# Optimization experiments

Measured on AMD Instinct MI355X. Metric: run time of the kernel, lower is better.

## Reference

```python
import jax, jax.numpy as jnp
import numpy as np

BN_EPS = 1e-5

def _conv3x3(x, w):
    # x: [N,C,H,W], w: [O,I,3,3], stride 1, padding 1, no bias
    return jax.lax.conv_general_dilated(
        x, w, window_strides=(1, 1), padding=((1, 1), (1, 1)),
        dimension_numbers=("NCHW", "OIHW", "NCHW"))

def _batchnorm(x, gamma, beta):
    # training-mode BN: batch statistics over (N,H,W)
    mean = jnp.mean(x, axis=(0, 2, 3), keepdims=True)
    var = jnp.mean(jnp.square(x - mean), axis=(0, 2, 3), keepdims=True)
    inv = jax.lax.rsqrt(var + BN_EPS)
    g = gamma.reshape(1, -1, 1, 1)
    b = beta.reshape(1, -1, 1, 1)
    return (x - mean) * inv * g + b

def setup_inputs() -> dict:
    key = jax.random.key(0)
    ks = jax.random.split(key, 3)
    x = jax.random.normal(ks[0], (32, 64, 128, 128), dtype=jnp.float32)
    # He-style scaled 3x3 conv kernels
    w1 = jax.random.normal(ks[1], (64, 64, 3, 3), dtype=jnp.float32) * (2.0 / (64 * 9)) ** 0.5
    w2 = jax.random.normal(ks[2], (64, 64, 3, 3), dtype=jnp.float32) * (2.0 / (64 * 9)) ** 0.5
    return {
        "x": x, "w1": w1, "w2": w2,
        "bn1_gamma": jnp.ones((64,), jnp.float32),
        "bn1_beta": jnp.zeros((64,), jnp.float32),
        "bn2_gamma": jnp.ones((64,), jnp.float32),
        "bn2_beta": jnp.zeros((64,), jnp.float32),
    }

def reference(x, w1, w2, bn1_gamma, bn1_beta, bn2_gamma, bn2_beta):
    out = _batchnorm(_conv3x3(x, w1), bn1_gamma, bn1_beta)
    out = _conv3x3(out, w2)
    out = out + x  # option 'A', stride=1, planes[2]==planes[0] -> identity shortcut
    return _batchnorm(out, bn2_gamma, bn2_beta)
```

## Files before the change

kernel.cpp:

```cpp
#include <hip/hip_runtime.h>
#include <hip/hip_bf16.h>

#define NB 32
#define CH 64
#define HH 128
#define WW 128
#define HW (HH*WW)
#define CHW (CH*HW)
#define NCHW (NB*CHW)
#define CNT_PER_CH ((float)(NB*HW))
#define SLOTS 256

typedef __attribute__((ext_vector_type(8)))  short short8;
typedef __attribute__((ext_vector_type(16))) float f32x16;

__device__ __forceinline__ unsigned short f2bf(float f) {
  unsigned u = __builtin_bit_cast(unsigned, f);
  u += 0x7fffu + ((u >> 16) & 1u);
  return (unsigned short)(u >> 16);
}

__global__ __launch_bounds__(256) void t1_pack(const float* __restrict__ x,
                                               unsigned short* __restrict__ xb) {
  __shared__ __align__(16) unsigned short tmp[CH * WW];
  const int bid = blockIdx.x;
  const int tid = threadIdx.x;
  const float* src = x + (size_t)(bid >> 7) * CHW + (size_t)(bid & 127) * WW;
  for (int i = tid; i < 2048; i += 256) {
    const int ci = i >> 5, wq = i & 31;
    const float4 v = *(const float4*)(src + (size_t)ci * HW + wq * 4);
    unsigned short* d = &tmp[ci * WW + wq * 4];
    d[0] = f2bf(v.x); d[1] = f2bf(v.y); d[2] = f2bf(v.z); d[3] = f2bf(v.w);
  }
  __syncthreads();
  unsigned short* dst = xb + (size_t)bid * 8192;
  for (int i = tid; i < 1024; i += 256) {
    const int cb = i >> 7, w = i & 127;
    const unsigned short* s = &tmp[cb * 8 * WW + w];
    uint4 o;
    o.x = (unsigned)s[0]      | ((unsigned)s[WW]     << 16);
    o.y = (unsigned)s[2*WW]   | ((unsigned)s[3*WW]   << 16);
    o.z = (unsigned)s[4*WW]   | ((unsigned)s[5*WW]   << 16);
    o.w = (unsigned)s[6*WW]   | ((unsigned)s[7*WW]   << 16);
    *(uint4*)(dst + ((size_t)cb * WW + w) * 8) = o;
  }
}

__global__ __launch_bounds__(256) void pack_w(const float* __restrict__ w,
                                              const float* __restrict__ s1,
                                              const float* __restrict__ b1,
                                              unsigned short* __restrict__ wpk,
                                              float* __restrict__ tabs) {
  const int tid = threadIdx.x;
  for (int idx = tid; idx < 36864; idx += 256) {
    const int f = idx >> 9, l = (idx >> 3) & 63, r = idx & 7;
    const int m = f & 1, kq = (f >> 1) & 3, t = f >> 3;
    const int co = (l & 31) + 32 * m;
    const int ci = kq * 16 + (l >> 5) * 8 + r;
    float v = w[co * 576 + ci * 9 + t];
    if (s1) v *= s1[ci];
    wpk[idx] = f2bf(v);
  }
  if (tabs != nullptr && tid < 64) {
    const int co = tid;
    float tb[9];
    for (int t = 0; t < 9; ++t) {
      float a = 0.f;
      for (int ci = 0; ci < 64; ++ci) a += w[co * 576 + ci * 9 + t] * b1[ci];
      tb[t] = a;
    }
    tabs[0*64+co] = tb[0]+tb[1]+tb[2]+tb[3]+tb[4]+tb[5]+tb[6]+tb[7]+tb[8];
    tabs[1*64+co] = tb[0]+tb[1]+tb[2];
    tabs[2*64+co] = tb[6]+tb[7]+tb[8];
    tabs[3*64+co] = tb[0]+tb[3]+tb[6];
    tabs[4*64+co] = tb[2]+tb[5]+tb[8];
    tabs[5*64+co] = tb[0]; tabs[6*64+co] = tb[2];
    tabs[7*64+co] = tb[6]; tabs[8*64+co] = tb[8];
  }
}

template <bool IS2>
__global__ __launch_bounds__(64, 3)
void conv_stream(const unsigned short* __restrict__ inb,
                 const unsigned short* __restrict__ wpack,
                 const float* __restrict__ tabs,
                 const float* __restrict__ resid,
                 unsigned short* __restrict__ outb,
                 float* __restrict__ outf,
                 float* __restrict__ psum, float* __restrict__ psq) {
  const int b = blockIdx.x;
  const int vid = ((b & 7) << 11) | (b >> 3);
  const int seg = vid & 3;
  const int h   = (vid >> 2) & 127;
  const int n   = vid >> 9;
  const int lane = threadIdx.x;
  const int half = lane >> 5, lp = lane & 31;
  const int px = (seg << 5) + lp;

  f32x16 acc0 = {}; f32x16 acc1 = {};
  const unsigned short* nbase = inb + (size_t)n * (128 * 8192);

#pragma unroll
  for (int kh = 0; kh < 3; ++kh) {
    const int hr = h + kh - 1;
    if ((unsigned)hr >= 128u) continue;
    const unsigned short* rb = nbase + (size_t)hr * 8192;
#pragma unroll
    for (int kw = 0; kw < 3; ++kw) {
      const int pxs = px + kw - 1;
      const bool wok = (unsigned)pxs < 128u;
      const int pxc = pxs < 0 ? 0 : (pxs > 127 ? 127 : pxs);
#pragma unroll
      for (int kq = 0; kq < 4; ++kq) {
        const int cb = (kq << 1) + half;
        short8 bf = *(const short8*)(rb + ((size_t)cb << 10) + ((size_t)pxc << 3));
        short8 zz = {};
        if (!wok) bf = zz;
        const int f = (((kh * 3 + kw) << 2) + kq) << 1;
        const short8 w0 = *(const short8*)(wpack + ((size_t)f << 9) + ((size_t)lane << 3));
        const short8 w1 = *(const short8*)(wpack + ((size_t)(f + 1) << 9) + ((size_t)lane << 3));
        acc0 = __builtin_amdgcn_mfma_f32_32x32x16_bf16(w0, bf, acc0, 0, 0, 0);
        acc1 = __builtin_amdgcn_mfma_f32_32x32x16_bf16(w1, bf, acc1, 0, 0, 0);
      }
    }
  }

  if (!IS2) {
    unsigned short* dst = outb + (size_t)(n * 128 + h) * 8192;
#pragma unroll
    for (int m = 0; m < 2; ++m) {
      const f32x16& a = m ? acc1 : acc0;
#pragma unroll
      for (int rq = 0; rq < 4; ++rq) {
        uint2 pk;
        pk.x = (unsigned)f2bf(a[rq*4+0]) | ((unsigned)f2bf(a[rq*4+1]) << 16);
        pk.y = (unsigned)f2bf(a[rq*4+2]) | ((unsigned)f2bf(a[rq*4+3]) << 16);
        *(uint2*)(dst + (((size_t)(rq + (m << 2))) << 10) + ((size_t)px << 3) + (half << 2)) = pk;
      }
    }
  } else {
    const bool bh0 = (h == 0), bh1 = (h == 127);
    const bool bw0 = (px == 0), bw1 = (px == 127);
#pragma unroll
    for (int m = 0; m < 2; ++m) {
      f32x16& a = m ? acc1 : acc0;
#pragma unroll
      for (int r = 0; r < 16; ++r) {
        const int co = (r & 3) + ((r >> 2) << 3) + (half << 2) + (m << 5);
        float tb = tabs[co];
        if (bh0) tb -= tabs[64 + co];
        if (bh1) tb -= tabs[128 + co];
        if (bw0) tb -= tabs[192 + co];
        if (bw1) tb -= tabs[256 + co];
        if (bh0 && bw0) tb += tabs[320 + co];
        if (bh0 && bw1) tb += tabs[384 + co];
        if (bh1 && bw0) tb += tabs[448 + co];
        if (bh1 && bw1) tb += tabs[512 + co];
        const size_t oi = (((size_t)(n * 64 + co)) * 128 + h) * 128 + px;
        const float v = a[r] + tb + resid[oi];
        outf[oi] = v;
        a[r] = v;
      }
    }
  }

  const int slot = vid & (SLOTS - 1);
#pragma unroll
  for (int m = 0; m < 2; ++m) {
    const f32x16& a = m ? acc1 : acc0;
#pragma unroll
    for (int r = 0; r < 16; ++r) {
      float s = a[r], q = a[r] * a[r];
      s += __shfl_xor(s, 1);  q += __shfl_xor(q, 1);
      s += __shfl_xor(s, 2);  q += __shfl_xor(q, 2);
      s += __shfl_xor(s, 4);  q += __shfl_xor(q, 4);
      s += __shfl_xor(s, 8);  q += __shfl_xor(q, 8);
      s += __shfl_xor(s, 16); q += __shfl_xor(q, 16);
      if (lp == 0) {
        const int co = (r & 3) + ((r >> 2) << 3) + (half << 2) + (m << 5);
        atomicAdd(&psum[slot * 64 + co], s);
        atomicAdd(&psq [slot * 64 + co], q);
      }
    }
  }
}

__global__ __launch_bounds__(256)
void finalize_bn(const float* __restrict__ psum, const float* __restrict__ psq,
                 const float* __restrict__ gamma, const float* __restrict__ beta,
                 float* __restrict__ scale, float* __restrict__ bias) {
  __shared__ float ls[4][64], lq[4][64];
  const int c = threadIdx.x & 63, sg = threadIdx.x >> 6;
  float s = 0.f, q = 0.f;
  for (int i = sg * (SLOTS / 4); i < (sg + 1) * (SLOTS / 4); ++i) {
    s += psum[(size_t)i * 64 + c];
    q += psq[(size_t)i * 64 + c];
  }
  ls[sg][c] = s; lq[sg][c] = q;
  __syncthreads();
  if (threadIdx.x < 64) {
    s = ls[0][c] + ls[1][c] + ls[2][c] + ls[3][c];
    q = lq[0][c] + lq[1][c] + lq[2][c] + lq[3][c];
    const float mean = s * (1.0f / CNT_PER_CH);
    const float var  = q * (1.0f / CNT_PER_CH) - mean * mean;
    const float inv  = rsqrtf(var + 1e-5f);
    const float sc   = inv * gamma[c];
    scale[c] = sc;
    bias[c]  = beta[c] - mean * sc;
  }
}

__global__ __launch_bounds__(256)
void apply_bn_k(float* __restrict__ out,
                const float* __restrict__ scale, const float* __restrict__ bias) {
  __shared__ float sc[CH], bs[CH];
  if (threadIdx.x < CH) { sc[threadIdx.x] = scale[threadIdx.x]; bs[threadIdx.x] = bias[threadIdx.x]; }
  __syncthreads();
  const size_t total4 = NCHW / 4;
  for (size_t i = (size_t)blockIdx.x * blockDim.x + threadIdx.x; i < total4;
       i += (size_t)gridDim.x * blockDim.x) {
    float4 v = reinterpret_cast<float4*>(out)[i];
    const int c = (int)(((i * 4) >> 14) & 63);
    const float s = sc[c], b = bs[c];
    v.x = fmaf(v.x, s, b);
    v.y = fmaf(v.y, s, b);
    v.z = fmaf(v.z, s, b);
    v.w = fmaf(v.w, s, b);
    reinterpret_cast<float4*>(out)[i] = v;
  }
}

extern "C" void kernel_launch(void* const* d_in, const int* in_sizes, int n_in,
                              void* d_out, int out_size, void* d_ws, size_t ws_size,
                              hipStream_t stream) {
  const float* x  = (const float*)d_in[0];
  const float* w1 = (const float*)d_in[1];
  const float* w2 = (const float*)d_in[2];
  const float* g1 = (const float*)d_in[3];
  const float* b1 = (const float*)d_in[4];
  const float* g2 = (const float*)d_in[5];
  const float* b2 = (const float*)d_in[6];
  float* out = (float*)d_out;
  char* ws = (char*)d_ws;

  unsigned short* XB  = (unsigned short*)ws;
  unsigned short* Y1B = (unsigned short*)(ws + 67108864);
  unsigned short* W2P = (unsigned short*)ws;
  float* TABS = (float*)(ws + 73728);
  float* SC1  = (float*)(ws + 76032);
  float* BS1  = (float*)(ws + 76288);
  float* SC2  = (float*)(ws + 76544);
  float* BS2  = (float*)(ws + 76800);
  float* P2S  = (float*)(ws + 131072);
  float* P2Q  = (float*)(ws + 131072 + 65536);
  char* ob = (char*)d_out;
  unsigned short* W1P = (unsigned short*)ob;
  float* P1S = (float*)(ob + 73728);
  float* P1Q = (float*)(ob + 73728 + 65536);

  pack_w<<<1, 256, 0, stream>>>(w1, nullptr, nullptr, W1P, nullptr);
  hipMemsetAsync(ob + 73728, 0, 131072, stream);
  t1_pack<<<4096, 256, 0, stream>>>(x, XB);
  conv_stream<false><<<16384, 64, 0, stream>>>(XB, W1P, nullptr, nullptr,
                                               Y1B, nullptr, P1S, P1Q);
  finalize_bn<<<1, 256, 0, stream>>>(P1S, P1Q, g1, b1, SC1, BS1);
  hipMemsetAsync(ws + 131072, 0, 131072, stream);
  pack_w<<<1, 256, 0, stream>>>(w2, SC1, BS1, W2P, TABS);
  conv_stream<true><<<16384, 64, 0, stream>>>(Y1B, W2P, TABS, x,
                                              nullptr, out, P2S, P2Q);
  finalize_bn<<<1, 256, 0, stream>>>(P2S, P2Q, g2, b2, SC2, BS2);
  apply_bn_k<<<2048, 256, 0, stream>>>(out, SC2, BS2);
}
```

Baseline: 550.9 us.

## Split conv waves by output-channel half and hold weights in registers

Each wave now computes one 32-channel half of the output over 64 pixels, instead of all 64 channels over 32 pixels. This lets the wave preload its 36 weight fragments into registers once rather than reloading weights from memory inside the inner loop. The BN statistics reduction combines both pixel groups before the shuffle tree, halving the shuffle and atomic work. In exchange, input tiles are read twice (once per channel half), register pressure rises, and the launch bound drops to 2 waves per SIMD, which lowers occupancy.

```diff
diff --git a/kernel.cpp b/kernel.cpp
--- a/kernel.cpp
+++ b/kernel.cpp
@@ -80,7 +80,7 @@
 }
 
 template <bool IS2>
-__global__ __launch_bounds__(64, 3)
+__global__ __launch_bounds__(64, 2)
 void conv_stream(const unsigned short* __restrict__ inb,
                  const unsigned short* __restrict__ wpack,
                  const float* __restrict__ tabs,
@@ -90,12 +90,22 @@
                  float* __restrict__ psum, float* __restrict__ psq) {
   const int b = blockIdx.x;
   const int vid = ((b & 7) << 11) | (b >> 3);
-  const int seg = vid & 3;
-  const int h   = (vid >> 2) & 127;
-  const int n   = vid >> 9;
+  const int h  = vid & 127;
+  const int g  = vid >> 7;
+  const int m  = g & 1;
+  const int sp = (g >> 1) & 1;
+  const int n  = g >> 2;
   const int lane = threadIdx.x;
   const int half = lane >> 5, lp = lane & 31;
-  const int px = (seg << 5) + lp;
+  const int px0 = (sp << 6) + lp;
+  const int px1 = px0 + 32;
+
+  short8 wr[36];
+#pragma unroll
+  for (int i = 0; i < 36; ++i) {
+    const int f = (i << 1) + m;
+    wr[i] = *(const short8*)(wpack + ((size_t)f << 9) + ((size_t)lane << 3));
+  }
 
   f32x16 acc0 = {}; f32x16 acc1 = {};
   const unsigned short* nbase = inb + (size_t)n * (128 * 8192);
@@ -107,20 +117,23 @@
     const unsigned short* rb = nbase + (size_t)hr * 8192;
 #pragma unroll
     for (int kw = 0; kw < 3; ++kw) {
-      const int pxs = px + kw - 1;
-      const bool wok = (unsigned)pxs < 128u;
-      const int pxc = pxs < 0 ? 0 : (pxs > 127 ? 127 : pxs);
+      const int p0 = px0 + kw - 1;
+      const int p1 = px1 + kw - 1;
+      const bool ok0 = (unsigned)p0 < 128u;
+      const bool ok1 = (unsigned)p1 < 128u;
+      const int c0 = p0 < 0 ? 0 : (p0 > 127 ? 127 : p0);
+      const int c1 = p1 < 0 ? 0 : (p1 > 127 ? 127 : p1);
 #pragma unroll
       for (int kq = 0; kq < 4; ++kq) {
         const int cb = (kq << 1) + half;
-        short8 bf = *(const short8*)(rb + ((size_t)cb << 10) + ((size_t)pxc << 3));
+        short8 b0 = *(const short8*)(rb + ((size_t)cb << 10) + ((size_t)c0 << 3));
+        short8 b1 = *(const short8*)(rb + ((size_t)cb << 10) + ((size_t)c1 << 3));
         short8 zz = {};
-        if (!wok) bf = zz;
-        const int f = (((kh * 3 + kw) << 2) + kq) << 1;
-        const short8 w0 = *(const short8*)(wpack + ((size_t)f << 9) + ((size_t)lane << 3));
-        const short8 w1 = *(const short8*)(wpack + ((size_t)(f + 1) << 9) + ((size_t)lane << 3));
-        acc0 = __builtin_amdgcn_mfma_f32_32x32x16_bf16(w0, bf, acc0, 0, 0, 0);
-        acc1 = __builtin_amdgcn_mfma_f32_32x32x16_bf16(w1, bf, acc1, 0, 0, 0);
+        if (!ok0) b0 = zz;
+        if (!ok1) b1 = zz;
+        const short8 wf = wr[(kh * 3 + kw) * 4 + kq];
+        acc0 = __builtin_amdgcn_mfma_f32_32x32x16_bf16(wf, b0, acc0, 0, 0, 0);
+        acc1 = __builtin_amdgcn_mfma_f32_32x32x16_bf16(wf, b1, acc1, 0, 0, 0);
       }
     }
   }
@@ -128,8 +141,9 @@
   if (!IS2) {
     unsigned short* dst = outb + (size_t)(n * 128 + h) * 8192;
 #pragma unroll
-    for (int m = 0; m < 2; ++m) {
-      const f32x16& a = m ? acc1 : acc0;
+    for (int s = 0; s < 2; ++s) {
+      const f32x16& a = s ? acc1 : acc0;
+      const int px = s ? px1 : px0;
 #pragma unroll
       for (int rq = 0; rq < 4; ++rq) {
         uint2 pk;
@@ -140,10 +154,11 @@
     }
   } else {
     const bool bh0 = (h == 0), bh1 = (h == 127);
-    const bool bw0 = (px == 0), bw1 = (px == 127);
-#pragma unroll
-    for (int m = 0; m < 2; ++m) {
-      f32x16& a = m ? acc1 : acc0;
+#pragma unroll
+    for (int s = 0; s < 2; ++s) {
+      f32x16& a = s ? acc1 : acc0;
+      const int px = s ? px1 : px0;
+      const bool bw0 = (px == 0), bw1 = (px == 127);
 #pragma unroll
       for (int r = 0; r < 16; ++r) {
         const int co = (r & 3) + ((r >> 2) << 3) + (half << 2) + (m << 5);
@@ -166,21 +181,18 @@
 
   const int slot = vid & (SLOTS - 1);
 #pragma unroll
-  for (int m = 0; m < 2; ++m) {
-    const f32x16& a = m ? acc1 : acc0;
-#pragma unroll
-    for (int r = 0; r < 16; ++r) {
-      float s = a[r], q = a[r] * a[r];
-      s += __shfl_xor(s, 1);  q += __shfl_xor(q, 1);
-      s += __shfl_xor(s, 2);  q += __shfl_xor(q, 2);
-      s += __shfl_xor(s, 4);  q += __shfl_xor(q, 4);
-      s += __shfl_xor(s, 8);  q += __shfl_xor(q, 8);
-      s += __shfl_xor(s, 16); q += __shfl_xor(q, 16);
-      if (lp == 0) {
-        const int co = (r & 3) + ((r >> 2) << 3) + (half << 2) + (m << 5);
-        atomicAdd(&psum[slot * 64 + co], s);
-        atomicAdd(&psq [slot * 64 + co], q);
-      }
+  for (int r = 0; r < 16; ++r) {
+    float s = acc0[r] + acc1[r];
+    float q = acc0[r] * acc0[r] + acc1[r] * acc1[r];
+    s += __shfl_xor(s, 1);  q += __shfl_xor(q, 1);
+    s += __shfl_xor(s, 2);  q += __shfl_xor(q, 2);
+    s += __shfl_xor(s, 4);  q += __shfl_xor(q, 4);
+    s += __shfl_xor(s, 8);  q += __shfl_xor(q, 8);
+    s += __shfl_xor(s, 16); q += __shfl_xor(q, 16);
+    if (lp == 0) {
+      const int co = (r & 3) + ((r >> 2) << 3) + (half << 2) + (m << 5);
+      atomicAdd(&psum[slot * 64 + co], s);
+      atomicAdd(&psq [slot * 64 + co], q);
     }
   }
 }
```

New measurement: 652.8 us. 18.5% more time.

## Tile conv over two output rows with LDS-staged input and register-resident weights

Applied to the files above, without the earlier changes.

Replaces the one-wave-per-32-pixel conv kernel with a 256-thread block that computes two full output rows. The four input rows it needs are staged into LDS using global_load_lds, and each wave keeps its half of the packed weights in registers. Every input fragment and weight then feeds four MFMAs instead of being reloaded from global memory per segment. The cost is heavy register pressure from 36 weight fragments plus 4 accumulators, a block-wide barrier, and fewer, larger blocks.

```diff
diff --git a/kernel.cpp b/kernel.cpp
--- a/kernel.cpp
+++ b/kernel.cpp
@@ -18,6 +18,12 @@
   unsigned u = __builtin_bit_cast(unsigned, f);
   u += 0x7fffu + ((u >> 16) & 1u);
   return (unsigned short)(u >> 16);
+}
+
+__device__ __forceinline__ void gld_lds16(const void* g, void* s) {
+  __builtin_amdgcn_global_load_lds(
+      (const __attribute__((address_space(1))) unsigned int*)g,
+      (__attribute__((address_space(3))) unsigned int*)s, 16, 0, 0);
 }
 
 __global__ __launch_bounds__(256) void t1_pack(const float* __restrict__ x,
@@ -80,56 +86,82 @@
 }
 
 template <bool IS2>
-__global__ __launch_bounds__(64, 3)
-void conv_stream(const unsigned short* __restrict__ inb,
-                 const unsigned short* __restrict__ wpack,
-                 const float* __restrict__ tabs,
-                 const float* __restrict__ resid,
-                 unsigned short* __restrict__ outb,
-                 float* __restrict__ outf,
-                 float* __restrict__ psum, float* __restrict__ psq) {
+__global__ __launch_bounds__(256, 2)
+void conv_tile(const unsigned short* __restrict__ inb,
+               const unsigned short* __restrict__ wpack,
+               const float* __restrict__ tabs,
+               const float* __restrict__ resid,
+               unsigned short* __restrict__ outb,
+               float* __restrict__ outf,
+               float* __restrict__ psum, float* __restrict__ psq) {
+  __shared__ __align__(16) unsigned short A[4][8][128][8];
   const int b = blockIdx.x;
-  const int vid = ((b & 7) << 11) | (b >> 3);
-  const int seg = vid & 3;
-  const int h   = (vid >> 2) & 127;
-  const int n   = vid >> 9;
-  const int lane = threadIdx.x;
+  const int vid = ((b & 7) << 8) | (b >> 3);
+  const int n  = vid >> 6;
+  const int h0 = (vid & 63) << 1;
+  const int tid = threadIdx.x;
+  const int wv = tid >> 6, lane = tid & 63;
   const int half = lane >> 5, lp = lane & 31;
-  const int px = (seg << 5) + lp;
-
-  f32x16 acc0 = {}; f32x16 acc1 = {};
-  const unsigned short* nbase = inb + (size_t)n * (128 * 8192);
-
+  const int m   = wv & 1;
+  const int row = wv >> 1;
+  const int rrow = h0 + row;
+
+  short8 wr[36];
+#pragma unroll
+  for (int i = 0; i < 36; ++i) {
+    const int f = (i << 1) + m;
+    wr[i] = *(const short8*)(wpack + ((size_t)f << 9) + ((size_t)lane << 3));
+  }
+
+#pragma unroll
+  for (int t = 0; t < 16; ++t) {
+    const int task = wv + (t << 2);
+    const int ri = task >> 4, cb = (task >> 1) & 7, wh = task & 1;
+    const int hr = h0 - 1 + ri;
+    if ((unsigned)hr < 128u) {
+      const unsigned short* g = inb + ((((size_t)n * 128 + hr) * 8 + cb) << 10)
+                                    + (size_t)((wh << 6) + lane) * 8;
+      gld_lds16(g, &A[ri][cb][wh << 6][0]);
+    } else {
+      *(uint4*)&A[ri][cb][(wh << 6) + lane][0] = make_uint4(0, 0, 0, 0);
+    }
+  }
+  __syncthreads();
+
+  f32x16 acc[4] = {{}, {}, {}, {}};
 #pragma unroll
   for (int kh = 0; kh < 3; ++kh) {
-    const int hr = h + kh - 1;
-    if ((unsigned)hr >= 128u) continue;
-    const unsigned short* rb = nbase + (size_t)hr * 8192;
+    const int ri = row + kh;
 #pragma unroll
     for (int kw = 0; kw < 3; ++kw) {
-      const int pxs = px + kw - 1;
-      const bool wok = (unsigned)pxs < 128u;
-      const int pxc = pxs < 0 ? 0 : (pxs > 127 ? 127 : pxs);
 #pragma unroll
       for (int kq = 0; kq < 4; ++kq) {
+        const short8 wf = wr[(kh * 3 + kw) * 4 + kq];
         const int cb = (kq << 1) + half;
-        short8 bf = *(const short8*)(rb + ((size_t)cb << 10) + ((size_t)pxc << 3));
-        short8 zz = {};
-        if (!wok) bf = zz;
-        const int f = (((kh * 3 + kw) << 2) + kq) << 1;
-        const short8 w0 = *(const short8*)(wpack + ((size_t)f << 9) + ((size_t)lane << 3));
-        const short8 w1 = *(const short8*)(wpack + ((size_t)(f + 1) << 9) + ((size_t)lane << 3));
-        acc0 = __builtin_amdgcn_mfma_f32_32x32x16_bf16(w0, bf, acc0, 0, 0, 0);
-        acc1 = __builtin_amdgcn_mfma_f32_32x32x16_bf16(w1, bf, acc1, 0, 0, 0);
+#pragma unroll
+        for (int seg = 0; seg < 4; ++seg) {
+          const int ps = (seg << 5) + lp + kw - 1;
+          int pc = ps;
+          bool zero = false;
+          if (kw == 0 && seg == 0) { pc = ps < 0 ? 0 : ps; zero = ps < 0; }
+          if (kw == 2 && seg == 3) { pc = ps > 127 ? 127 : ps; zero = ps > 127; }
+          short8 bf = *(const short8*)&A[ri][cb][pc][0];
+          if ((kw == 0 && seg == 0) || (kw == 2 && seg == 3)) {
+            short8 zz = {};
+            if (zero) bf = zz;
+          }
+          acc[seg] = __builtin_amdgcn_mfma_f32_32x32x16_bf16(wf, bf, acc[seg], 0, 0, 0);
+        }
       }
     }
   }
 
   if (!IS2) {
-    unsigned short* dst = outb + (size_t)(n * 128 + h) * 8192;
-#pragma unroll
-    for (int m = 0; m < 2; ++m) {
-      const f32x16& a = m ? acc1 : acc0;
+    unsigned short* dst = outb + (size_t)(n * 128 + rrow) * 8192;
+#pragma unroll
+    for (int seg = 0; seg < 4; ++seg) {
+      const f32x16& a = acc[seg];
+      const int px = (seg << 5) + lp;
 #pragma unroll
       for (int rq = 0; rq < 4; ++rq) {
         uint2 pk;
@@ -139,11 +171,12 @@
       }
     }
   } else {
-    const bool bh0 = (h == 0), bh1 = (h == 127);
-    const bool bw0 = (px == 0), bw1 = (px == 127);
-#pragma unroll
-    for (int m = 0; m < 2; ++m) {
-      f32x16& a = m ? acc1 : acc0;
+    const bool bh0 = (rrow == 0), bh1 = (rrow == 127);
+#pragma unroll
+    for (int seg = 0; seg < 4; ++seg) {
+      f32x16& a = acc[seg];
+      const int px = (seg << 5) + lp;
+      const bool bw0 = (px == 0), bw1 = (px == 127);
 #pragma unroll
       for (int r = 0; r < 16; ++r) {
         const int co = (r & 3) + ((r >> 2) << 3) + (half << 2) + (m << 5);
@@ -156,7 +189,7 @@
         if (bh0 && bw1) tb += tabs[384 + co];
         if (bh1 && bw0) tb += tabs[448 + co];
         if (bh1 && bw1) tb += tabs[512 + co];
-        const size_t oi = (((size_t)(n * 64 + co)) * 128 + h) * 128 + px;
+        const size_t oi = (((size_t)(n * 64 + co)) * 128 + rrow) * 128 + px;
         const float v = a[r] + tb + resid[oi];
         outf[oi] = v;
         a[r] = v;
@@ -166,21 +199,19 @@
 
   const int slot = vid & (SLOTS - 1);
 #pragma unroll
-  for (int m = 0; m < 2; ++m) {
-    const f32x16& a = m ? acc1 : acc0;
-#pragma unroll
-    for (int r = 0; r < 16; ++r) {
-      float s = a[r], q = a[r] * a[r];
-      s += __shfl_xor(s, 1);  q += __shfl_xor(q, 1);
-      s += __shfl_xor(s, 2);  q += __shfl_xor(q, 2);
-      s += __shfl_xor(s, 4);  q += __shfl_xor(q, 4);
-      s += __shfl_xor(s, 8);  q += __shfl_xor(q, 8);
-      s += __shfl_xor(s, 16); q += __shfl_xor(q, 16);
-      if (lp == 0) {
-        const int co = (r & 3) + ((r >> 2) << 3) + (half << 2) + (m << 5);
-        atomicAdd(&psum[slot * 64 + co], s);
-        atomicAdd(&psq [slot * 64 + co], q);
-      }
+  for (int r = 0; r < 16; ++r) {
+    float s = acc[0][r] + acc[1][r] + acc[2][r] + acc[3][r];
+    float q = acc[0][r]*acc[0][r] + acc[1][r]*acc[1][r]
+            + acc[2][r]*acc[2][r] + acc[3][r]*acc[3][r];
+    s += __shfl_xor(s, 1);  q += __shfl_xor(q, 1);
+    s += __shfl_xor(s, 2);  q += __shfl_xor(q, 2);
+    s += __shfl_xor(s, 4);  q += __shfl_xor(q, 4);
+    s += __shfl_xor(s, 8);  q += __shfl_xor(q, 8);
+    s += __shfl_xor(s, 16); q += __shfl_xor(q, 16);
+    if (lp == 0) {
+      const int co = (r & 3) + ((r >> 2) << 3) + (half << 2) + (m << 5);
+      atomicAdd(&psum[slot * 64 + co], s);
+      atomicAdd(&psq [slot * 64 + co], q);
     }
   }
 }
@@ -261,13 +292,13 @@
   pack_w<<<1, 256, 0, stream>>>(w1, nullptr, nullptr, W1P, nullptr);
   hipMemsetAsync(ob + 73728, 0, 131072, stream);
   t1_pack<<<4096, 256, 0, stream>>>(x, XB);
-  conv_stream<false><<<16384, 64, 0, stream>>>(XB, W1P, nullptr, nullptr,
-                                               Y1B, nullptr, P1S, P1Q);
+  conv_tile<false><<<2048, 256, 0, stream>>>(XB, W1P, nullptr, nullptr,
+                                             Y1B, nullptr, P1S, P1Q);
   finalize_bn<<<1, 256, 0, stream>>>(P1S, P1Q, g1, b1, SC1, BS1);
   hipMemsetAsync(ws + 131072, 0, 131072, stream);
   pack_w<<<1, 256, 0, stream>>>(w2, SC1, BS1, W2P, TABS);
-  conv_stream<true><<<16384, 64, 0, stream>>>(Y1B, W2P, TABS, x,
-                                              nullptr, out, P2S, P2Q);
+  conv_tile<true><<<2048, 256, 0, stream>>>(Y1B, W2P, TABS, x,
+                                            nullptr, out, P2S, P2Q);
   finalize_bn<<<1, 256, 0, stream>>>(P2S, P2Q, g2, b2, SC2, BS2);
   apply_bn_k<<<2048, 256, 0, stream>>>(out, SC2, BS2);
 }
```

Measured after the change: 573.9 us. 1.04x slower.
